# Optimization experiments

Hardware: AMD Instinct MI355X
Metric: run time of the kernel (lower is better)

Reference implementation:

```python
import jax, jax.numpy as jnp
import numpy as np

V, OOV, E, HE, HD, B, S, T = 50000, 100, 128, 256, 256, 32, 256, 16
NEG = -1e20


def lstm(x, W, U, b, h0, c0):
    # x: [B, L, F]; standard (Keras-style i,f,g,o) LSTM via scan over time
    def step(carry, xt):
        h, c = carry
        z = xt @ W + h @ U + b
        i, f, g, o = jnp.split(z, 4, axis=-1)
        c = jax.nn.sigmoid(f) * c + jax.nn.sigmoid(i) * jnp.tanh(g)
        h = jax.nn.sigmoid(o) * jnp.tanh(c)
        return (h, c), h
    (h, c), hs = jax.lax.scan(step, (h0, c0), jnp.swapaxes(x, 0, 1))
    return jnp.swapaxes(hs, 0, 1), h, c


def setup_inputs() -> dict:
    key = jax.random.key(0)
    ks = jax.random.split(key, 16)
    g = lambda i, shape: jax.random.normal(ks[i], shape, dtype=jnp.float32) * 0.05
    return {
        'x': jax.random.randint(ks[0], (B, S), 0, V),
        'x_with_oov': jax.random.randint(ks[1], (B, S), 0, V + OOV),
        'x_len': jax.random.randint(ks[2], (B,), 1, S + 1),
        'dec_x': jax.random.randint(ks[3], (B, T), 0, V),
        'embedding': g(4, (V, E)),
        'Wenc': g(5, (E, 4 * HE)), 'Uenc': g(6, (HE, 4 * HE)), 'benc': jnp.zeros(4 * HE, jnp.float32),
        'We2d': g(7, (HE, HD)), 'be2d': jnp.zeros(HD, jnp.float32),
        'Wdec': g(8, (E, 4 * HD)), 'Udec': g(9, (HD, 4 * HD)), 'bdec': jnp.zeros(4 * HD, jnp.float32),
        'Wattn': g(10, (HD, HE)),
        'Wout': g(11, (HE + HD, HD)), 'bout': jnp.zeros(HD, jnp.float32),
        'Wgen': g(12, (HD, V)),
        'Wcopy': g(13, (HE, HD)), 'bcopy': jnp.zeros(HD, jnp.float32),
    }


def reference(x, x_with_oov, x_len, dec_x, embedding, Wenc, Uenc, benc,
              We2d, be2d, Wdec, Udec, bdec, Wattn, Wout, bout, Wgen, Wcopy, bcopy):
    # Encoder (unidirectional; Keras encoder ignores mask in this branch)
    enc_out, eh, ec = lstm(embedding[x], Wenc, Uenc, benc,
                           jnp.zeros((B, HE), embedding.dtype), jnp.zeros((B, HE), embedding.dtype))
    # NOTE: source applies encoder2decoder_state to BOTH h and c (faithful)
    h0 = eh @ We2d + be2d
    c0 = ec @ We2d + be2d
    # Decoder LSTM
    dec_out, sh, sc = lstm(embedding[dec_x], Wdec, Udec, bdec, h0, c0)  # [B,T,HD]
    mask = jnp.arange(S)[None, :] < x_len[:, None]                      # [B,S]
    # Attention (score_mode='general')
    scores = jnp.einsum('bth,he,bse->bts', dec_out, Wattn, enc_out)     # [B,T,S]
    scores = jnp.where(mask[:, None, :], scores, NEG)
    aw = jax.nn.softmax(scores, axis=2)
    ctx = jnp.einsum('bts,bse->bte', aw, enc_out)                       # [B,T,HE]
    attn_out = jnp.tanh(jnp.concatenate([ctx, dec_out], axis=-1) @ Wout + bout)  # [B,T,HD]
    # Generation scores, padded with tiny constant over OOV slots
    gen = jnp.exp(attn_out @ Wgen)                                      # [B,T,V]
    gen = jnp.pad(gen, ((0, 0), (0, 0), (0, OOV)), constant_values=1e-10)
    # Copy scores over source positions, scattered into extended vocab
    copy_seq = jnp.einsum('bsh,bth->bts', jnp.tanh(enc_out @ Wcopy + bcopy), attn_out)
    copy_seq = jnp.exp(jnp.where(mask[:, None, :], copy_seq, NEG))      # [B,T,S]
    b_idx = jnp.arange(B)[:, None, None]
    t_idx = jnp.arange(T)[None, :, None]
    v_idx = x_with_oov[:, None, :]                                      # broadcast to [B,T,S]
    copy_vocab = jnp.zeros((B, T, V + OOV), gen.dtype).at[b_idx, t_idx, v_idx].add(copy_seq)
    total = gen + copy_vocab
    log_prob = jnp.log(total / jnp.sum(total, axis=2, keepdims=True))
    return log_prob, sh, sc
```

## Files before the change

### kernel.cpp

```cpp
#include <hip/hip_runtime.h>

#define V_   50000
#define OOV_ 100
#define VO_  50100
#define E_   128
#define HE_  256
#define HD_  256
#define B_   32
#define S_   256
#define T_   16

typedef _Float16 h2_t __attribute__((ext_vector_type(2)));
typedef __attribute__((ext_vector_type(8))) short bfrag_t;
typedef __attribute__((ext_vector_type(4))) float f32x4;
typedef unsigned short ushort_t;

union U32H2 { unsigned u; h2_t h; };
union FRAG  { uint4 u; bfrag_t s; };

static __device__ __forceinline__ float bf2f(unsigned short b) {
  return __uint_as_float(((unsigned)b) << 16);
}
static __device__ __forceinline__ unsigned short f2bf(float f) {
  unsigned u = __float_as_uint(f);
  unsigned r = (u + 0x7fffu + ((u >> 16) & 1u)) >> 16;
  return (unsigned short)r;
}
static __device__ __forceinline__ float sigm(float x) { return 1.f / (1.f + expf(-x)); }

static __device__ __forceinline__ float dot2u(unsigned upair, unsigned hpairv, float acc) {
  U32H2 a; a.u = upair;
  U32H2 b; b.u = hpairv;
#if __has_builtin(__builtin_amdgcn_fdot2)
  return __builtin_amdgcn_fdot2(a.h, b.h, acc, false);
#else
  acc = fmaf((float)a.h.x, (float)b.h.x, acc);
  return fmaf((float)a.h.y, (float)b.h.y, acc);
#endif
}

__global__ __launch_bounds__(256) void mfma_gemm(
    const ushort_t* __restrict__ A, const ushort_t* __restrict__ Bt,
    const float* __restrict__ bias, float* __restrict__ C, ushort_t* __restrict__ Cbf,
    float* __restrict__ rsum, int M, int N, int K, int ldC, int act)
{
  const int w = threadIdx.x >> 6, lane = threadIdx.x & 63;
  const int m0 = blockIdx.y * 64 + w * 16;
  const int n0 = blockIdx.x * 64;
  const int l16 = lane & 15, lq = lane >> 4;
  f32x4 acc[4] = {f32x4{0,0,0,0}, f32x4{0,0,0,0}, f32x4{0,0,0,0}, f32x4{0,0,0,0}};
  for (int k0 = 0; k0 < K; k0 += 32) {
    FRAG a;
    a.u = *(const uint4*)(A + (size_t)(m0 + l16) * K + k0 + lq * 8);
#pragma unroll
    for (int ns = 0; ns < 4; ns++) {
      int n = n0 + ns * 16 + l16;
      int nc = n < N ? n : N - 1;
      FRAG bf;
      bf.u = *(const uint4*)(Bt + (size_t)nc * K + k0 + lq * 8);
      acc[ns] = __builtin_amdgcn_mfma_f32_16x16x32_bf16(a.s, bf.s, acc[ns], 0, 0, 0);
    }
  }
  float bv[4];
#pragma unroll
  for (int ns = 0; ns < 4; ns++) {
    int col = n0 + ns * 16 + l16;
    bv[ns] = (bias && col < N) ? bias[col] : 0.f;
  }
#pragma unroll
  for (int r = 0; r < 4; r++) {
    int row = m0 + lq * 4 + r;
    float part = 0.f;
#pragma unroll
    for (int ns = 0; ns < 4; ns++) {
      int col = n0 + ns * 16 + l16;
      if (col < N) {
        float v = acc[ns][r] + bv[ns];
        if (act == 1) v = tanhf(v);
        else if (act == 2) v = expf(v);
        if (Cbf) Cbf[(size_t)row * ldC + col] = f2bf(v);
        else     C[(size_t)row * ldC + col] = v;
        part += v;
      }
    }
    if (rsum) {
      part += __shfl_xor(part, 1);
      part += __shfl_xor(part, 2);
      part += __shfl_xor(part, 4);
      part += __shfl_xor(part, 8);
      if (l16 == 0) atomicAdd(&rsum[row], part);
    }
  }
}

static __device__ __forceinline__ void tconv_tile(
    const float* __restrict__ W, ushort_t* __restrict__ Wt, int K, int N,
    int kb, int nb, int tid, ushort_t (*tile)[33])
{
  const int tx = tid & 31, ty = tid >> 5;
#pragma unroll
  for (int p = 0; p < 4; p++) {
    int k = kb + ty + p * 8, n = nb + tx;
    if (k < K && n < N) tile[ty + p * 8][tx] = f2bf(W[(size_t)k * N + n]);
  }
  __syncthreads();
#pragma unroll
  for (int p = 0; p < 4; p++) {
    int n = nb + ty + p * 8, k = kb + tx;
    if (k < K && n < N) Wt[(size_t)n * K + k] = tile[tx][ty + p * 8];
  }
}
static __device__ __forceinline__ void packU2_one(
    const float* __restrict__ U, unsigned* __restrict__ out, int i)
{
  int p = i >> 10, col = i & 1023;
  U32H2 cv; cv.h = h2_t{(_Float16)U[(size_t)(2 * p) * 1024 + col],
                        (_Float16)U[(size_t)(2 * p + 1) * 1024 + col]};
  out[i] = cv.u;
}

__global__ __launch_bounds__(256) void prep_kernel(
    const float* __restrict__ Wenc, const float* __restrict__ Wdec,
    const float* __restrict__ We2d, const float* __restrict__ Wattn,
    const float* __restrict__ Wout, const float* __restrict__ Wcopy,
    const float* __restrict__ Uenc, const float* __restrict__ Udec,
    const int* __restrict__ x, const int* __restrict__ decx, const float* __restrict__ emb,
    ushort_t* WencT, ushort_t* WdecT, ushort_t* We2dT, ushort_t* WattnT,
    ushort_t* WoutT, ushort_t* WcopyT, unsigned* Upk2E, unsigned* Upk2D,
    ushort_t* xembbf, ushort_t* dembbf)
{
  __shared__ ushort_t tile[32][33];
  int blk = blockIdx.x;
  const int tid = threadIdx.x;
  if (blk < 128) { tconv_tile(Wenc, WencT, 128, 1024, (blk >> 5) * 32, (blk & 31) * 32, tid, tile); return; }
  blk -= 128;
  if (blk < 128) { tconv_tile(Wdec, WdecT, 128, 1024, (blk >> 5) * 32, (blk & 31) * 32, tid, tile); return; }
  blk -= 128;
  if (blk < 64)  { tconv_tile(We2d, We2dT, 256, 256, (blk >> 3) * 32, (blk & 7) * 32, tid, tile); return; }
  blk -= 64;
  if (blk < 64)  { tconv_tile(Wattn, WattnT, 256, 256, (blk >> 3) * 32, (blk & 7) * 32, tid, tile); return; }
  blk -= 64;
  if (blk < 128) { tconv_tile(Wout, WoutT, 512, 256, (blk >> 3) * 32, (blk & 7) * 32, tid, tile); return; }
  blk -= 128;
  if (blk < 64)  { tconv_tile(Wcopy, WcopyT, 256, 256, (blk >> 3) * 32, (blk & 7) * 32, tid, tile); return; }
  blk -= 64;
  if (blk < 512) { packU2_one(Uenc, Upk2E, blk * 256 + tid); return; }
  blk -= 512;
  if (blk < 512) { packU2_one(Udec, Upk2D, blk * 256 + tid); return; }
  blk -= 512;
  if (blk < 4096) {
    int i = blk * 256 + tid, r = i >> 7;
    xembbf[i] = f2bf(emb[(size_t)x[r] * E_ + (i & 127)]);
    return;
  }
  blk -= 4096;
  {
    int i = blk * 256 + tid, r = i >> 7;
    dembbf[i] = f2bf(emb[(size_t)decx[r] * E_ + (i & 127)]);
  }
}

#define DOT8(u0, u1, hpi)                \
  acc[0] = dot2u(u0.x, hpi, acc[0]);     \
  acc[1] = dot2u(u0.y, hpi, acc[1]);     \
  acc[2] = dot2u(u0.z, hpi, acc[2]);     \
  acc[3] = dot2u(u0.w, hpi, acc[3]);     \
  acc[4] = dot2u(u1.x, hpi, acc[4]);     \
  acc[5] = dot2u(u1.y, hpi, acc[5]);     \
  acc[6] = dot2u(u1.z, hpi, acc[6]);     \
  acc[7] = dot2u(u1.w, hpi, acc[7]);

__global__ __launch_bounds__(1024, 4) void lstm4(
    const float* __restrict__ Xpre, const unsigned* __restrict__ Upk2,
    const float* __restrict__ h0, const float* __restrict__ c0,
    ushort_t* __restrict__ outH, float* __restrict__ hN, float* __restrict__ cN,
    int steps, const float* __restrict__ Wg, ushort_t* __restrict__ WgT)
{
  __shared__ unsigned ldsU[32 * 1028];
  __shared__ float zpart[4 * 1028];
  __shared__ float actbuf[1024];
  __shared__ unsigned hpair[128];
  const int tid = threadIdx.x;

  if (blockIdx.x >= 32) {
    ushort_t* tile = (ushort_t*)ldsU;
    int tb = blockIdx.x - 32;
    int kb = (tb & 3) * 64, nb = (tb >> 2) * 64;
#pragma unroll
    for (int p = 0; p < 4; p++) {
      int i = p * 1024 + tid, k = i >> 6, n = i & 63;
      if (nb + n < V_) tile[k * 65 + n] = f2bf(Wg[(size_t)(kb + k) * V_ + nb + n]);
    }
    __syncthreads();
#pragma unroll
    for (int p = 0; p < 4; p++) {
      int i = p * 1024 + tid, n = i >> 6, k = i & 63;
      if (nb + n < V_) WgT[(size_t)(nb + n) * 256 + kb + k] = tile[k * 65 + n];
    }
    return;
  }

  const int b = blockIdx.x;
  const int jg = tid >> 3, kq = tid & 7;

  uint4 Ur[24];
  const unsigned* ubase = Upk2 + jg * 8;
#pragma unroll
  for (int i = 0; i < 12; i++) {
    int p = kq * 16 + i;
    Ur[2 * i]     = *(const uint4*)(ubase + p * 1024);
    Ur[2 * i + 1] = *(const uint4*)(ubase + p * 1024 + 4);
  }
#pragma unroll
  for (int i = 0; i < 4; i++) {
    int p = kq * 16 + 12 + i;
    uint4 q0 = *(const uint4*)(ubase + p * 1024);
    uint4 q1 = *(const uint4*)(ubase + p * 1024 + 4);
    *(uint4*)&ldsU[(kq * 4 + i) * 1028 + jg * 8] = q0;
    *(uint4*)&ldsU[(kq * 4 + i) * 1028 + jg * 8 + 4] = q1;
  }
  float c = 0.f, hcur = 0.f;
  if (tid < 256) {
    c    = c0 ? c0[b * 256 + tid] : 0.f;
    hcur = h0 ? h0[b * 256 + tid] : 0.f;
  }
  if (tid < 128) {
    float a  = h0 ? h0[b * 256 + 2 * tid] : 0.f;
    float b2 = h0 ? h0[b * 256 + 2 * tid + 1] : 0.f;
    U32H2 cv; cv.h = h2_t{(_Float16)a, (_Float16)b2};
    hpair[tid] = cv.u;
  }
  __syncthreads();

  const float* xp = Xpre + (size_t)b * steps * 1024;
  const unsigned* myld = &ldsU[kq * 4 * 1028 + jg * 8];

  for (int t = 0; t < steps; t++) {
    float xv = xp[t * 1024 + tid];
    float acc[8] = {0.f, 0.f, 0.f, 0.f, 0.f, 0.f, 0.f, 0.f};
    {
      uint4 hA = *(const uint4*)&hpair[kq * 16];
      DOT8(Ur[0], Ur[1], hA.x)  DOT8(Ur[2], Ur[3], hA.y)
      DOT8(Ur[4], Ur[5], hA.z)  DOT8(Ur[6], Ur[7], hA.w)
    }
    {
      uint4 hB = *(const uint4*)&hpair[kq * 16 + 4];
      DOT8(Ur[8], Ur[9], hB.x)   DOT8(Ur[10], Ur[11], hB.y)
      DOT8(Ur[12], Ur[13], hB.z) DOT8(Ur[14], Ur[15], hB.w)
    }
    {
      uint4 hC = *(const uint4*)&hpair[kq * 16 + 8];
      DOT8(Ur[16], Ur[17], hC.x) DOT8(Ur[18], Ur[19], hC.y)
      DOT8(Ur[20], Ur[21], hC.z) DOT8(Ur[22], Ur[23], hC.w)
    }
    {
      uint4 hD = *(const uint4*)&hpair[kq * 16 + 12];
      unsigned hh[4] = {hD.x, hD.y, hD.z, hD.w};
#pragma unroll
      for (int r = 0; r < 4; r++) {
        uint4 u0 = *(const uint4*)(myld + r * 1028);
        uint4 u1 = *(const uint4*)(myld + r * 1028 + 4);
        unsigned hpi = hh[r];
        DOT8(u0, u1, hpi)
      }
    }
#pragma unroll
    for (int g = 0; g < 8; g++) acc[g] += __shfl_xor(acc[g], 1);
    if ((kq & 1) == 0) {
      int r = kq >> 1;
      *(float4*)&zpart[r * 1028 + jg * 8]     = make_float4(acc[0], acc[1], acc[2], acc[3]);
      *(float4*)&zpart[r * 1028 + jg * 8 + 4] = make_float4(acc[4], acc[5], acc[6], acc[7]);
    }
    __syncthreads();
    float z = xv + zpart[tid] + zpart[1028 + tid] + zpart[2 * 1028 + tid] + zpart[3 * 1028 + tid];
    actbuf[tid] = (tid >= 512 && tid < 768) ? tanhf(z) : sigm(z);
    __syncthreads();
    if (tid < 256) {
      float ai = actbuf[tid], af = actbuf[tid + 256];
      float gg = actbuf[tid + 512], ao = actbuf[tid + 768];
      c = af * c + ai * gg;
      hcur = ao * tanhf(c);
      outH[((size_t)b * steps + t) * 256 + tid] = f2bf(hcur);
      float hnx = __shfl_down(hcur, 1);
      if ((tid & 1) == 0) {
        U32H2 cv; cv.h = h2_t{(_Float16)hcur, (_Float16)hnx};
        hpair[tid >> 1] = cv.u;
      }
    }
    __syncthreads();
  }
  if (tid < 256) {
    hN[b * 256 + tid] = hcur;
    cN[b * 256 + tid] = c;
  }
}

__global__ __launch_bounds__(256) void attn_kernel(
    const float* __restrict__ dq, const ushort_t* __restrict__ enc,
    const int* __restrict__ x_len, float* __restrict__ ctx)
{
  __shared__ float q[256];
  __shared__ float eb[32][256];
  __shared__ float sc[256];
  __shared__ float red[8];
  const int bt = blockIdx.x, tid = threadIdx.x;
  const int b = bt >> 4;
  q[tid] = dq[(size_t)bt * 256 + tid];
  const int len = x_len[b];
  const unsigned* encu = (const unsigned*)(enc + (size_t)b * S_ * 256);
  __syncthreads();
  const int s_loc = tid >> 3, hb = (tid & 7) * 32;
  for (int cch = 0; cch < 8; cch++) {
#pragma unroll
    for (int qv = 0; qv < 16; qv++) {
      int idx = qv * 256 + tid;
      unsigned u = encu[cch * 4096 + idx];
      int row = idx >> 7, cp2 = (idx & 127) * 2;
      eb[row][cp2]     = bf2f((unsigned short)(u & 0xffffu));
      eb[row][cp2 + 1] = bf2f((unsigned short)(u >> 16));
    }
    __syncthreads();
    float p = 0.f;
#pragma unroll
    for (int h = 0; h < 32; h++) p = fmaf(q[hb + h], eb[s_loc][hb + h], p);
    p += __shfl_down(p, 4, 8);
    p += __shfl_down(p, 2, 8);
    p += __shfl_down(p, 1, 8);
    if ((tid & 7) == 0) sc[cch * 32 + s_loc] = p;
    __syncthreads();
  }
  float my = (tid < len) ? sc[tid] : -1e30f;
  float m = my;
#pragma unroll
  for (int o = 32; o >= 1; o >>= 1) m = fmaxf(m, __shfl_xor(m, o));
  if ((tid & 63) == 0) red[tid >> 6] = m;
  __syncthreads();
  float bm = fmaxf(fmaxf(red[0], red[1]), fmaxf(red[2], red[3]));
  float e = expf(my - bm);
  float s = e;
#pragma unroll
  for (int o = 32; o >= 1; o >>= 1) s += __shfl_xor(s, o);
  if ((tid & 63) == 0) red[4 + (tid >> 6)] = s;
  __syncthreads();
  float tot = red[4] + red[5] + red[6] + red[7];
  sc[tid] = e / tot;
  __syncthreads();
  const ushort_t* encb = enc + (size_t)b * S_ * 256;
// ... 78 lines not shown
  size_t i = (size_t)blockIdx.x * 256 + threadIdx.x;
  if (i < (size_t)B_ * T_ * VO_) {
    int bt = (int)(i / VO_);
    out[i] = logf(out[i]) - rowlog[bt];
  }
}

extern "C" void kernel_launch(void* const* d_in, const int* in_sizes, int n_in,
                              void* d_out, int out_size, void* d_ws, size_t ws_size,
                              hipStream_t stream) {
  const int*   x     = (const int*)d_in[0];
  const int*   xoov  = (const int*)d_in[1];
  const int*   xlen  = (const int*)d_in[2];
  const int*   decx  = (const int*)d_in[3];
  const float* emb   = (const float*)d_in[4];
  const float* Wenc  = (const float*)d_in[5];
  const float* Uenc  = (const float*)d_in[6];
  const float* benc  = (const float*)d_in[7];
  const float* We2d  = (const float*)d_in[8];
  const float* be2d  = (const float*)d_in[9];
  const float* Wdec  = (const float*)d_in[10];
  const float* Udec  = (const float*)d_in[11];
  const float* bdec  = (const float*)d_in[12];
  const float* Wattn = (const float*)d_in[13];
  const float* Wout  = (const float*)d_in[14];
  const float* bout  = (const float*)d_in[15];
  const float* Wgen  = (const float*)d_in[16];
  const float* Wcopy = (const float*)d_in[17];
  const float* bcopy = (const float*)d_in[18];
  float* out = (float*)d_out;
  float* ws  = (float*)d_ws;

  float*    Xenc   = ws + 0;
  ushort_t* WgenT  = (ushort_t*)(ws + 0);
  ushort_t* cp_bf  = (ushort_t*)(ws + 6400000);
  float*    dqb    = ws + 8388608;
  float*    ctxb   = ws + 8519680;
  float*    attno  = ws + 8650752;
  float*    cseq   = ws + 8781824;
  float*    rsum   = ws + 8912896;
  float*    rowlog = ws + 8913408;
  ushort_t* Abf    = (ushort_t*)(ws + 8913920);
  ushort_t* catb   = (ushort_t*)(ws + 8979456);
  ushort_t* decObf = (ushort_t*)(ws + 9110528);
  ushort_t* xembbf = (ushort_t*)(ws + 9176064);
  ushort_t* dembbf = (ushort_t*)(ws + 9700352);
  float*    Xdec   = ws + 9733120;
  ushort_t* WencT  = (ushort_t*)(ws + 10257408);
  ushort_t* WdecT  = (ushort_t*)(ws + 10322944);
  ushort_t* We2dT  = (ushort_t*)(ws + 10388480);
  ushort_t* WattnT = (ushort_t*)(ws + 10421248);
  ushort_t* WoutT  = (ushort_t*)(ws + 10454016);
  ushort_t* WcopyT = (ushort_t*)(ws + 10519552);
  unsigned* Upk2E  = (unsigned*)(ws + 10552320);
  unsigned* Upk2D  = (unsigned*)(ws + 10683392);
  ushort_t* encObf = (ushort_t*)(ws + 10814464);
  float*    ehc    = ws + 11863040;
  ushort_t* ehcbf  = (ushort_t*)(ws + 11879424);
  float*    h0c0   = ws + 11887616;

  float* sh  = out + (size_t)B_ * T_ * VO_;
  float* scf = sh + B_ * HD_;

  hipMemsetAsync(rsum, 0, 512 * sizeof(float), stream);

  hipLaunchKernelGGL(prep_kernel, dim3(5952), dim3(256), 0, stream,
                     Wenc, Wdec, We2d, Wattn, Wout, Wcopy, Uenc, Udec, x, decx, emb,
                     WencT, WdecT, We2dT, WattnT, WoutT, WcopyT, Upk2E, Upk2D,
                     xembbf, dembbf);

  hipLaunchKernelGGL(mfma_gemm, dim3(16, 128), dim3(256), 0, stream,
                     xembbf, WencT, benc, Xenc, (ushort_t*)nullptr, (float*)nullptr,
                     B_ * S_, 1024, 128, 1024, 0);
  hipLaunchKernelGGL(mfma_gemm, dim3(16, 8), dim3(256), 0, stream,
                     dembbf, WdecT, bdec, Xdec, (ushort_t*)nullptr, (float*)nullptr,
                     B_ * T_, 1024, 128, 1024, 0);

  hipLaunchKernelGGL(lstm4, dim3(32), dim3(1024), 0, stream,
                     Xenc, Upk2E, (const float*)nullptr, (const float*)nullptr,
                     encObf, ehc, ehc + 32 * 256, S_,
                     (const float*)nullptr, (ushort_t*)nullptr);

  hipLaunchKernelGGL(f2bf_kernel, dim3(64), dim3(256), 0, stream, ehc, ehcbf, 64 * 256);
  hipLaunchKernelGGL(mfma_gemm, dim3(4, 1), dim3(256), 0, stream,
                     ehcbf, We2dT, be2d, h0c0, (ushort_t*)nullptr, (float*)nullptr,
                     64, 256, 256, 256, 0);

  hipLaunchKernelGGL(lstm4, dim3(32 + 3128), dim3(1024), 0, stream,
                     Xdec, Upk2D, h0c0, h0c0 + 32 * 256, decObf, sh, scf, T_,
                     Wgen, WgenT);

  hipLaunchKernelGGL(mfma_gemm, dim3(4, 8), dim3(256), 0, stream,
                     decObf, WattnT, (const float*)nullptr, dqb, (ushort_t*)nullptr,
                     (float*)nullptr, B_ * T_, 256, 256, 256, 0);
  hipLaunchKernelGGL(attn_kernel, dim3(B_ * T_), dim3(256), 0, stream, dqb, encObf, xlen, ctxb);
  hipLaunchKernelGGL(concat_bf, dim3(1024), dim3(256), 0, stream, ctxb, decObf, catb);
  hipLaunchKernelGGL(mfma_gemm, dim3(4, 8), dim3(256), 0, stream,
                     catb, WoutT, bout, attno, (ushort_t*)nullptr, (float*)nullptr,
                     B_ * T_, 256, 512, 256, 1);
  hipLaunchKernelGGL(f2bf_kernel, dim3(512), dim3(256), 0, stream, attno, Abf, B_ * T_ * 256);
  hipLaunchKernelGGL(mfma_gemm, dim3(4, 128), dim3(256), 0, stream,
                     encObf, WcopyT, bcopy, (float*)nullptr, cp_bf, (float*)nullptr,
                     B_ * S_, 256, 256, 256, 1);
  hipLaunchKernelGGL(mfma_gemm, dim3(782, 8), dim3(256), 0, stream,
                     Abf, WgenT, (const float*)nullptr, out, (ushort_t*)nullptr, rsum,
                     B_ * T_, V_, 256, VO_, 2);
  hipLaunchKernelGGL(pad_kernel, dim3(200), dim3(256), 0, stream, out);
  hipLaunchKernelGGL(copyseq_kernel, dim3(B_ * T_), dim3(256), 0, stream, attno, cp_bf, xlen, cseq);
  hipLaunchKernelGGL(scatter_kernel, dim3(512), dim3(256), 0, stream, cseq, xoov, out, rsum);
  hipLaunchKernelGGL(rowlog_kernel, dim3(2), dim3(256), 0, stream, rsum, rowlog);
  hipLaunchKernelGGL(finalize_kernel, dim3((B_ * T_ * VO_ + 255) / 256), dim3(256), 0, stream,
                     out, rowlog);
}
```

Baseline: 1.215 ms.

## Restructure LSTM recurrence so each thread group owns all four gates of a unit

Repacks the recurrent weight matrix so a quad of threads holds the i/f/g/o columns for one hidden unit, with each thread covering a quarter of the K range. Partial sums are reduced with quad shuffles and the cell update is done in registers, which removes the zpart/actbuf shared-memory round trips. A double-buffered h array cuts the per-step barriers from two to one. tanh is replaced by an exp-based formula, which trades a little accuracy for fewer instructions.

```diff
diff --git a/kernel.cpp b/kernel.cpp
--- a/kernel.cpp
+++ b/kernel.cpp
@@ -27,6 +27,9 @@
   return (unsigned short)r;
 }
 static __device__ __forceinline__ float sigm(float x) { return 1.f / (1.f + expf(-x)); }
+static __device__ __forceinline__ float tanh_fast(float x) {
+  return 2.f / (1.f + expf(-2.f * x)) - 1.f;
+}
 
 static __device__ __forceinline__ float dot2u(unsigned upair, unsigned hpairv, float acc) {
   U32H2 a; a.u = upair;
@@ -113,7 +116,8 @@
 static __device__ __forceinline__ void packU2_one(
     const float* __restrict__ U, unsigned* __restrict__ out, int i)
 {
-  int p = i >> 10, col = i & 1023;
+  int q = i & 3, g = (i >> 2) & 255, p = i >> 10;
+  int col = q * 256 + g;
   U32H2 cv; cv.h = h2_t{(_Float16)U[(size_t)(2 * p) * 1024 + col],
                         (_Float16)U[(size_t)(2 * p + 1) * 1024 + col]};
   out[i] = cv.u;
@@ -160,26 +164,20 @@
   }
 }
 
-#define DOT8(u0, u1, hpi)                \
-  acc[0] = dot2u(u0.x, hpi, acc[0]);     \
-  acc[1] = dot2u(u0.y, hpi, acc[1]);     \
-  acc[2] = dot2u(u0.z, hpi, acc[2]);     \
-  acc[3] = dot2u(u0.w, hpi, acc[3]);     \
-  acc[4] = dot2u(u1.x, hpi, acc[4]);     \
-  acc[5] = dot2u(u1.y, hpi, acc[5]);     \
-  acc[6] = dot2u(u1.z, hpi, acc[6]);     \
-  acc[7] = dot2u(u1.w, hpi, acc[7]);
-
-__global__ __launch_bounds__(1024, 4) void lstm4(
-    const float* __restrict__ Xpre, const unsigned* __restrict__ Upk2,
+#define PSTEP(Uv, hv)                       \
+  acc0 = dot2u((Uv).x, hv, acc0);           \
+  acc1 = dot2u((Uv).y, hv, acc1);           \
+  acc2 = dot2u((Uv).z, hv, acc2);           \
+  acc3 = dot2u((Uv).w, hv, acc3);
+
+__global__ __launch_bounds__(1024, 4) void lstm5(
+    const float* __restrict__ Xpre, const unsigned* __restrict__ Upk,
     const float* __restrict__ h0, const float* __restrict__ c0,
     ushort_t* __restrict__ outH, float* __restrict__ hN, float* __restrict__ cN,
     int steps, const float* __restrict__ Wg, ushort_t* __restrict__ WgT)
 {
-  __shared__ unsigned ldsU[32 * 1028];
-  __shared__ float zpart[4 * 1028];
-  __shared__ float actbuf[1024];
-  __shared__ unsigned hpair[128];
+  __shared__ unsigned ldsU[8 * 4096];
+  __shared__ unsigned hbuf[2][4 * 36];
   const int tid = threadIdx.x;
 
   if (blockIdx.x >= 32) {
@@ -201,97 +199,73 @@
   }
 
   const int b = blockIdx.x;
-  const int jg = tid >> 3, kq = tid & 7;
+  const int g = tid >> 2, r = tid & 3;
 
   uint4 Ur[24];
-  const unsigned* ubase = Upk2 + jg * 8;
-#pragma unroll
-  for (int i = 0; i < 12; i++) {
-    int p = kq * 16 + i;
-    Ur[2 * i]     = *(const uint4*)(ubase + p * 1024);
-    Ur[2 * i + 1] = *(const uint4*)(ubase + p * 1024 + 4);
-  }
-#pragma unroll
-  for (int i = 0; i < 4; i++) {
-    int p = kq * 16 + 12 + i;
-    uint4 q0 = *(const uint4*)(ubase + p * 1024);
-    uint4 q1 = *(const uint4*)(ubase + p * 1024 + 4);
-    *(uint4*)&ldsU[(kq * 4 + i) * 1028 + jg * 8] = q0;
-    *(uint4*)&ldsU[(kq * 4 + i) * 1028 + jg * 8 + 4] = q1;
-  }
-  float c = 0.f, hcur = 0.f;
-  if (tid < 256) {
-    c    = c0 ? c0[b * 256 + tid] : 0.f;
-    hcur = h0 ? h0[b * 256 + tid] : 0.f;
-  }
+  const unsigned* ub = Upk + ((size_t)(r * 32) * 256 + g) * 4;
+#pragma unroll
+  for (int j = 0; j < 24; j++) Ur[j] = *(const uint4*)(ub + j * 1024);
+#pragma unroll
+  for (int j = 0; j < 8; j++)
+    *(uint4*)&ldsU[j * 4096 + tid * 4] = *(const uint4*)(ub + (24 + j) * 1024);
+
+  float c = c0 ? c0[b * 256 + g] : 0.f;
+  float hcur = 0.f;
   if (tid < 128) {
-    float a  = h0 ? h0[b * 256 + 2 * tid] : 0.f;
+    float a  = h0 ? h0[b * 256 + 2 * tid]     : 0.f;
     float b2 = h0 ? h0[b * 256 + 2 * tid + 1] : 0.f;
     U32H2 cv; cv.h = h2_t{(_Float16)a, (_Float16)b2};
-    hpair[tid] = cv.u;
-  }
-  __syncthreads();
-
-  const float* xp = Xpre + (size_t)b * steps * 1024;
-  const unsigned* myld = &ldsU[kq * 4 * 1028 + jg * 8];
-
+    hbuf[0][(tid >> 5) * 36 + (tid & 31)] = cv.u;
+  }
+  __syncthreads();
+
+  const float* xp = Xpre + (size_t)b * steps * 1024 + r * 256 + g;
+  const unsigned* myld = &ldsU[tid * 4];
+
+  int cur = 0;
   for (int t = 0; t < steps; t++) {
-    float xv = xp[t * 1024 + tid];
-    float acc[8] = {0.f, 0.f, 0.f, 0.f, 0.f, 0.f, 0.f, 0.f};
-    {
-      uint4 hA = *(const uint4*)&hpair[kq * 16];
-      DOT8(Ur[0], Ur[1], hA.x)  DOT8(Ur[2], Ur[3], hA.y)
-      DOT8(Ur[4], Ur[5], hA.z)  DOT8(Ur[6], Ur[7], hA.w)
-    }
-    {
-      uint4 hB = *(const uint4*)&hpair[kq * 16 + 4];
-      DOT8(Ur[8], Ur[9], hB.x)   DOT8(Ur[10], Ur[11], hB.y)
-      DOT8(Ur[12], Ur[13], hB.z) DOT8(Ur[14], Ur[15], hB.w)
-    }
-    {
-      uint4 hC = *(const uint4*)&hpair[kq * 16 + 8];
-      DOT8(Ur[16], Ur[17], hC.x) DOT8(Ur[18], Ur[19], hC.y)
-      DOT8(Ur[20], Ur[21], hC.z) DOT8(Ur[22], Ur[23], hC.w)
-    }
-    {
-      uint4 hD = *(const uint4*)&hpair[kq * 16 + 12];
-      unsigned hh[4] = {hD.x, hD.y, hD.z, hD.w};
-#pragma unroll
-      for (int r = 0; r < 4; r++) {
-        uint4 u0 = *(const uint4*)(myld + r * 1028);
-        uint4 u1 = *(const uint4*)(myld + r * 1028 + 4);
-        unsigned hpi = hh[r];
-        DOT8(u0, u1, hpi)
-      }
-    }
-#pragma unroll
-    for (int g = 0; g < 8; g++) acc[g] += __shfl_xor(acc[g], 1);
-    if ((kq & 1) == 0) {
-      int r = kq >> 1;
-      *(float4*)&zpart[r * 1028 + jg * 8]     = make_float4(acc[0], acc[1], acc[2], acc[3]);
-      *(float4*)&zpart[r * 1028 + jg * 8 + 4] = make_float4(acc[4], acc[5], acc[6], acc[7]);
-    }
+    float xv = xp[(size_t)t * 1024];
+    const unsigned* hb = &hbuf[cur][0] + r * 36;
+    float acc0 = 0.f, acc1 = 0.f, acc2 = 0.f, acc3 = 0.f;
+#pragma unroll
+    for (int cc = 0; cc < 6; cc++) {
+      uint4 hp = *(const uint4*)(hb + cc * 4);
+      PSTEP(Ur[4 * cc + 0], hp.x)
+      PSTEP(Ur[4 * cc + 1], hp.y)
+      PSTEP(Ur[4 * cc + 2], hp.z)
+      PSTEP(Ur[4 * cc + 3], hp.w)
+    }
+#pragma unroll
+    for (int j = 0; j < 8; j++) {
+      unsigned hv = hb[24 + j];
+      uint4 uv = *(const uint4*)(myld + j * 4096);
+      PSTEP(uv, hv)
+    }
+    acc0 += (r == 0) ? xv : 0.f;
+    acc1 += (r == 1) ? xv : 0.f;
+    acc2 += (r == 2) ? xv : 0.f;
+    acc3 += (r == 3) ? xv : 0.f;
+    acc0 += __shfl_xor(acc0, 1); acc0 += __shfl_xor(acc0, 2);
+    acc1 += __shfl_xor(acc1, 1); acc1 += __shfl_xor(acc1, 2);
+    acc2 += __shfl_xor(acc2, 1); acc2 += __shfl_xor(acc2, 2);
+    acc3 += __shfl_xor(acc3, 1); acc3 += __shfl_xor(acc3, 2);
+    float ci = sigm(acc0), cf = sigm(acc1);
+    float cg = tanh_fast(acc2), co = sigm(acc3);
+    c = cf * c + ci * cg;
+    hcur = co * tanh_fast(c);
+    if (r == 0) outH[((size_t)b * steps + t) * 256 + g] = f2bf(hcur);
+    float hn = __shfl_down(hcur, 4);
+    if ((tid & 7) == 0) {
+      U32H2 cv; cv.h = h2_t{(_Float16)hcur, (_Float16)hn};
+      int m = tid >> 3;
+      hbuf[cur ^ 1][(m >> 5) * 36 + (m & 31)] = cv.u;
+    }
+    cur ^= 1;
     __syncthreads();
-    float z = xv + zpart[tid] + zpart[1028 + tid] + zpart[2 * 1028 + tid] + zpart[3 * 1028 + tid];
-    actbuf[tid] = (tid >= 512 && tid < 768) ? tanhf(z) : sigm(z);
-    __syncthreads();
-    if (tid < 256) {
-      float ai = actbuf[tid], af = actbuf[tid + 256];
-      float gg = actbuf[tid + 512], ao = actbuf[tid + 768];
-      c = af * c + ai * gg;
-      hcur = ao * tanhf(c);
-      outH[((size_t)b * steps + t) * 256 + tid] = f2bf(hcur);
-      float hnx = __shfl_down(hcur, 1);
-      if ((tid & 1) == 0) {
-        U32H2 cv; cv.h = h2_t{(_Float16)hcur, (_Float16)hnx};
-        hpair[tid >> 1] = cv.u;
-      }
-    }
-    __syncthreads();
-  }
-  if (tid < 256) {
-    hN[b * 256 + tid] = hcur;
-    cN[b * 256 + tid] = c;
+  }
+  if (r == 0) {
+    hN[b * 256 + g] = hcur;
+    cN[b * 256 + g] = c;
   }
 }
 
@@ -501,7 +475,7 @@
                      dembbf, WdecT, bdec, Xdec, (ushort_t*)nullptr, (float*)nullptr,
                      B_ * T_, 1024, 128, 1024, 0);
 
-  hipLaunchKernelGGL(lstm4, dim3(32), dim3(1024), 0, stream,
+  hipLaunchKernelGGL(lstm5, dim3(32), dim3(1024), 0, stream,
                      Xenc, Upk2E, (const float*)nullptr, (const float*)nullptr,
                      encObf, ehc, ehc + 32 * 256, S_,
                      (const float*)nullptr, (ushort_t*)nullptr);
@@ -511,7 +485,7 @@
                      ehcbf, We2dT, be2d, h0c0, (ushort_t*)nullptr, (float*)nullptr,
                      64, 256, 256, 256, 0);
 
-  hipLaunchKernelGGL(lstm4, dim3(32 + 3128), dim3(1024), 0, stream,
+  hipLaunchKernelGGL(lstm5, dim3(32 + 3128), dim3(1024), 0, stream,
                      Xdec, Upk2D, h0c0, h0c0 + 32 * 256, decObf, sh, scf, T_,
                      Wgen, WgenT);
 
```

Result: slower. 1.347 ms (+10.8%).

## Replace dot2 LSTM recurrence with fp16 MFMA over fragment-packed U

Applied to the files above, without the earlier changes.

The per-step h@U product in the LSTM kernel moves from packed fdot2 accumulation with cross-lane shuffles and an LDS partial-sum reduction onto 16x16x32 fp16 MFMA. U is pre-packed into MFMA B-fragment layout, with part held in registers, part in LDS and the rest streamed from global memory each step. The change also prefetches the next step's input pre-activation and swaps expf/tanhf for exp2/rcp approximations. This removes the zpart reduction and a barrier per step, but re-reads part of U from global/L2 every step and broadcasts the batch-1 h vector across MFMA rows, wasting most of each MFMA.

```diff
diff --git a/kernel.cpp b/kernel.cpp
--- a/kernel.cpp
+++ b/kernel.cpp
@@ -12,11 +12,13 @@
 
 typedef _Float16 h2_t __attribute__((ext_vector_type(2)));
 typedef __attribute__((ext_vector_type(8))) short bfrag_t;
+typedef _Float16 hfrag_t __attribute__((ext_vector_type(8)));
 typedef __attribute__((ext_vector_type(4))) float f32x4;
 typedef unsigned short ushort_t;
 
 union U32H2 { unsigned u; h2_t h; };
 union FRAG  { uint4 u; bfrag_t s; };
+union FRAGH { uint4 u; hfrag_t h; };
 
 static __device__ __forceinline__ float bf2f(unsigned short b) {
   return __uint_as_float(((unsigned)b) << 16);
@@ -26,18 +28,10 @@
   unsigned r = (u + 0x7fffu + ((u >> 16) & 1u)) >> 16;
   return (unsigned short)r;
 }
+static __device__ __forceinline__ ushort_t f2h(float f) {
+  union { _Float16 h; ushort_t u; } cv; cv.h = (_Float16)f; return cv.u;
+}
 static __device__ __forceinline__ float sigm(float x) { return 1.f / (1.f + expf(-x)); }
-
-static __device__ __forceinline__ float dot2u(unsigned upair, unsigned hpairv, float acc) {
-  U32H2 a; a.u = upair;
-  U32H2 b; b.u = hpairv;
-#if __has_builtin(__builtin_amdgcn_fdot2)
-  return __builtin_amdgcn_fdot2(a.h, b.h, acc, false);
-#else
-  acc = fmaf((float)a.h.x, (float)b.h.x, acc);
-  return fmaf((float)a.h.y, (float)b.h.y, acc);
-#endif
-}
 
 __global__ __launch_bounds__(256) void mfma_gemm(
     const ushort_t* __restrict__ A, const ushort_t* __restrict__ Bt,
@@ -110,13 +104,13 @@
     if (k < K && n < N) Wt[(size_t)n * K + k] = tile[tx][ty + p * 8];
   }
 }
-static __device__ __forceinline__ void packU2_one(
-    const float* __restrict__ U, unsigned* __restrict__ out, int i)
-{
-  int p = i >> 10, col = i & 1023;
-  U32H2 cv; cv.h = h2_t{(_Float16)U[(size_t)(2 * p) * 1024 + col],
-                        (_Float16)U[(size_t)(2 * p + 1) * 1024 + col]};
-  out[i] = cv.u;
+static __device__ __forceinline__ void packUfrag_one(
+    const float* __restrict__ U, ushort_t* __restrict__ out, int i)
+{
+  int e = i & 7, l = (i >> 3) & 63, ntg = (i >> 9) & 63, kk = i >> 15;
+  int col = ntg * 16 + (l & 15);
+  int k = kk * 32 + (l >> 4) * 8 + e;
+  out[i] = f2h(U[(size_t)k * 1024 + col]);
 }
 
 __global__ __launch_bounds__(256) void prep_kernel(
@@ -126,7 +120,7 @@
     const float* __restrict__ Uenc, const float* __restrict__ Udec,
     const int* __restrict__ x, const int* __restrict__ decx, const float* __restrict__ emb,
     ushort_t* WencT, ushort_t* WdecT, ushort_t* We2dT, ushort_t* WattnT,
-    ushort_t* WoutT, ushort_t* WcopyT, unsigned* Upk2E, unsigned* Upk2D,
+    ushort_t* WoutT, ushort_t* WcopyT, ushort_t* UfragE, ushort_t* UfragD,
     ushort_t* xembbf, ushort_t* dembbf)
 {
   __shared__ ushort_t tile[32][33];
@@ -144,10 +138,10 @@
   blk -= 128;
   if (blk < 64)  { tconv_tile(Wcopy, WcopyT, 256, 256, (blk >> 3) * 32, (blk & 7) * 32, tid, tile); return; }
   blk -= 64;
-  if (blk < 512) { packU2_one(Uenc, Upk2E, blk * 256 + tid); return; }
-  blk -= 512;
-  if (blk < 512) { packU2_one(Udec, Upk2D, blk * 256 + tid); return; }
-  blk -= 512;
+  if (blk < 1024) { packUfrag_one(Uenc, UfragE, blk * 256 + tid); return; }
+  blk -= 1024;
+  if (blk < 1024) { packUfrag_one(Udec, UfragD, blk * 256 + tid); return; }
+  blk -= 1024;
   if (blk < 4096) {
     int i = blk * 256 + tid, r = i >> 7;
     xembbf[i] = f2bf(emb[(size_t)x[r] * E_ + (i & 127)]);
@@ -160,30 +154,19 @@
   }
 }
 
-#define DOT8(u0, u1, hpi)                \
-  acc[0] = dot2u(u0.x, hpi, acc[0]);     \
-  acc[1] = dot2u(u0.y, hpi, acc[1]);     \
-  acc[2] = dot2u(u0.z, hpi, acc[2]);     \
-  acc[3] = dot2u(u0.w, hpi, acc[3]);     \
-  acc[4] = dot2u(u1.x, hpi, acc[4]);     \
-  acc[5] = dot2u(u1.y, hpi, acc[5]);     \
-  acc[6] = dot2u(u1.z, hpi, acc[6]);     \
-  acc[7] = dot2u(u1.w, hpi, acc[7]);
-
-__global__ __launch_bounds__(1024, 4) void lstm4(
-    const float* __restrict__ Xpre, const unsigned* __restrict__ Upk2,
+__global__ __launch_bounds__(1024, 4) void lstm6(
+    const float* __restrict__ Xpre, const ushort_t* __restrict__ Ufrag,
     const float* __restrict__ h0, const float* __restrict__ c0,
     ushort_t* __restrict__ outH, float* __restrict__ hN, float* __restrict__ cN,
     int steps, const float* __restrict__ Wg, ushort_t* __restrict__ WgT)
 {
-  __shared__ unsigned ldsU[32 * 1028];
-  __shared__ float zpart[4 * 1028];
-  __shared__ float actbuf[1024];
-  __shared__ unsigned hpair[128];
+  __shared__ __align__(16) ushort_t ldsB[2 * 64 * 64 * 8];
+  __shared__ float actb[1024];
+  __shared__ __align__(16) ushort_t hH[256];
   const int tid = threadIdx.x;
 
   if (blockIdx.x >= 32) {
-    ushort_t* tile = (ushort_t*)ldsU;
+    ushort_t* tile = ldsB;
     int tb = blockIdx.x - 32;
     int kb = (tb & 3) * 64, nb = (tb >> 2) * 64;
 #pragma unroll
@@ -201,98 +184,105 @@
   }
 
   const int b = blockIdx.x;
-  const int jg = tid >> 3, kq = tid & 7;
-
-  uint4 Ur[24];
-  const unsigned* ubase = Upk2 + jg * 8;
-#pragma unroll
-  for (int i = 0; i < 12; i++) {
-    int p = kq * 16 + i;
-    Ur[2 * i]     = *(const uint4*)(ubase + p * 1024);
-    Ur[2 * i + 1] = *(const uint4*)(ubase + p * 1024 + 4);
-  }
-#pragma unroll
-  for (int i = 0; i < 4; i++) {
-    int p = kq * 16 + 12 + i;
-    uint4 q0 = *(const uint4*)(ubase + p * 1024);
-    uint4 q1 = *(const uint4*)(ubase + p * 1024 + 4);
-    *(uint4*)&ldsU[(kq * 4 + i) * 1028 + jg * 8] = q0;
-    *(uint4*)&ldsU[(kq * 4 + i) * 1028 + jg * 8 + 4] = q1;
-  }
+  const int w = tid >> 6, l = tid & 63;
+  const int lq = l >> 4, lq8 = lq * 8, w4 = w * 4;
+
+  const ushort_t* p0 = Ufrag + (size_t)w4 * 512 + l * 8;
+
+  FRAGH Br[12];
+#pragma unroll
+  for (int kk = 0; kk < 3; kk++)
+#pragma unroll
+    for (int j = 0; j < 4; j++)
+      Br[kk * 4 + j].u = *(const uint4*)(p0 + kk * 32768 + j * 512);
+#pragma unroll
+  for (int kk = 3; kk < 5; kk++)
+#pragma unroll
+    for (int j = 0; j < 4; j++) {
+      uint4 v = *(const uint4*)(p0 + kk * 32768 + j * 512);
+      *(uint4*)&ldsB[(size_t)(((kk - 3) * 64 + w4 + j) * 64 + l) * 8] = v;
+    }
+
   float c = 0.f, hcur = 0.f;
   if (tid < 256) {
     c    = c0 ? c0[b * 256 + tid] : 0.f;
     hcur = h0 ? h0[b * 256 + tid] : 0.f;
-  }
-  if (tid < 128) {
-    float a  = h0 ? h0[b * 256 + 2 * tid] : 0.f;
-    float b2 = h0 ? h0[b * 256 + 2 * tid + 1] : 0.f;
-    U32H2 cv; cv.h = h2_t{(_Float16)a, (_Float16)b2};
-    hpair[tid] = cv.u;
-  }
-  __syncthreads();
-
+    hH[tid] = f2h(hcur);
+  }
   const float* xp = Xpre + (size_t)b * steps * 1024;
-  const unsigned* myld = &ldsU[kq * 4 * 1028 + jg * 8];
+  float xv = xp[tid];
+  __syncthreads();
+
+#define KK_MFMA(KKI, B0, B1, B2, B3)                                              \
+  { FRAGH ah_; ah_.u = *(const uint4*)&hH[(KKI) * 32 + lq8];                      \
+    acc0 = __builtin_amdgcn_mfma_f32_16x16x32_f16(ah_.h, (B0).h, acc0, 0, 0, 0);  \
+    acc1 = __builtin_amdgcn_mfma_f32_16x16x32_f16(ah_.h, (B1).h, acc1, 0, 0, 0);  \
+    acc2 = __builtin_amdgcn_mfma_f32_16x16x32_f16(ah_.h, (B2).h, acc2, 0, 0, 0);  \
+    acc3 = __builtin_amdgcn_mfma_f32_16x16x32_f16(ah_.h, (B3).h, acc3, 0, 0, 0); }
 
   for (int t = 0; t < steps; t++) {
-    float xv = xp[t * 1024 + tid];
-    float acc[8] = {0.f, 0.f, 0.f, 0.f, 0.f, 0.f, 0.f, 0.f};
+    float xvn = xp[(size_t)((t + 1 < steps) ? t + 1 : t) * 1024 + tid];
+    f32x4 acc0 = f32x4{0,0,0,0}, acc1 = f32x4{0,0,0,0},
+          acc2 = f32x4{0,0,0,0}, acc3 = f32x4{0,0,0,0};
+    FRAGH g5[4], g6[4], g7[4];
+#pragma unroll
+    for (int j = 0; j < 4; j++) g5[j].u = *(const uint4*)(p0 + 5 * 32768 + j * 512);
+#pragma unroll
+    for (int j = 0; j < 4; j++) g6[j].u = *(const uint4*)(p0 + 6 * 32768 + j * 512);
+    KK_MFMA(0, Br[0], Br[1], Br[2], Br[3])
+    KK_MFMA(1, Br[4], Br[5], Br[6], Br[7])
+    KK_MFMA(2, Br[8], Br[9], Br[10], Br[11])
+    KK_MFMA(5, g5[0], g5[1], g5[2], g5[3])
+#pragma unroll
+    for (int j = 0; j < 4; j++) g7[j].u = *(const uint4*)(p0 + 7 * 32768 + j * 512);
+    KK_MFMA(6, g6[0], g6[1], g6[2], g6[3])
     {
-      uint4 hA = *(const uint4*)&hpair[kq * 16];
-      DOT8(Ur[0], Ur[1], hA.x)  DOT8(Ur[2], Ur[3], hA.y)
-      DOT8(Ur[4], Ur[5], hA.z)  DOT8(Ur[6], Ur[7], hA.w)
-    }
+      FRAGH b0, b1, b2, b3;
+      b0.u = *(const uint4*)&ldsB[(size_t)((0 * 64 + w4 + 0) * 64 + l) * 8];
+      b1.u = *(const uint4*)&ldsB[(size_t)((0 * 64 + w4 + 1) * 64 + l) * 8];
+      b2.u = *(const uint4*)&ldsB[(size_t)((0 * 64 + w4 + 2) * 64 + l) * 8];
+      b3.u = *(const uint4*)&ldsB[(size_t)((0 * 64 + w4 + 3) * 64 + l) * 8];
+      KK_MFMA(3, b0, b1, b2, b3)
+    }
+    KK_MFMA(7, g7[0], g7[1], g7[2], g7[3])
     {
-      uint4 hB = *(const uint4*)&hpair[kq * 16 + 4];
-      DOT8(Ur[8], Ur[9], hB.x)   DOT8(Ur[10], Ur[11], hB.y)
-      DOT8(Ur[12], Ur[13], hB.z) DOT8(Ur[14], Ur[15], hB.w)
-    }
-    {
-      uint4 hC = *(const uint4*)&hpair[kq * 16 + 8];
-      DOT8(Ur[16], Ur[17], hC.x) DOT8(Ur[18], Ur[19], hC.y)
-      DOT8(Ur[20], Ur[21], hC.z) DOT8(Ur[22], Ur[23], hC.w)
-    }
-    {
-      uint4 hD = *(const uint4*)&hpair[kq * 16 + 12];
-      unsigned hh[4] = {hD.x, hD.y, hD.z, hD.w};
-#pragma unroll
-      for (int r = 0; r < 4; r++) {
-        uint4 u0 = *(const uint4*)(myld + r * 1028);
-        uint4 u1 = *(const uint4*)(myld + r * 1028 + 4);
-        unsigned hpi = hh[r];
-        DOT8(u0, u1, hpi)
-      }
-    }
-#pragma unroll
-    for (int g = 0; g < 8; g++) acc[g] += __shfl_xor(acc[g], 1);
-    if ((kq & 1) == 0) {
-      int r = kq >> 1;
-      *(float4*)&zpart[r * 1028 + jg * 8]     = make_float4(acc[0], acc[1], acc[2], acc[3]);
-      *(float4*)&zpart[r * 1028 + jg * 8 + 4] = make_float4(acc[4], acc[5], acc[6], acc[7]);
-    }
-    __syncthreads();
-    float z = xv + zpart[tid] + zpart[1028 + tid] + zpart[2 * 1028 + tid] + zpart[3 * 1028 + tid];
-    actbuf[tid] = (tid >= 512 && tid < 768) ? tanhf(z) : sigm(z);
+      FRAGH b0, b1, b2, b3;
+      b0.u = *(const uint4*)&ldsB[(size_t)((1 * 64 + w4 + 0) * 64 + l) * 8];
+      b1.u = *(const uint4*)&ldsB[(size_t)((1 * 64 + w4 + 1) * 64 + l) * 8];
+      b2.u = *(const uint4*)&ldsB[(size_t)((1 * 64 + w4 + 2) * 64 + l) * 8];
+      b3.u = *(const uint4*)&ldsB[(size_t)((1 * 64 + w4 + 3) * 64 + l) * 8];
+      KK_MFMA(4, b0, b1, b2, b3)
+    }
+    float z = (lq == 0) ? acc0[0] : (lq == 1) ? acc1[0] : (lq == 2) ? acc2[0] : acc3[0];
+    z += xv;
+    float av;
+    if (w >= 8 && w < 12) {
+      float e = __builtin_amdgcn_exp2f(-2.885390082f * z);
+      av = 2.f * __builtin_amdgcn_rcpf(1.f + e) - 1.f;
+    } else {
+      float e = __builtin_amdgcn_exp2f(-1.442695041f * z);
+      av = __builtin_amdgcn_rcpf(1.f + e);
+    }
+    actb[tid] = av;
     __syncthreads();
     if (tid < 256) {
-      float ai = actbuf[tid], af = actbuf[tid + 256];
-      float gg = actbuf[tid + 512], ao = actbuf[tid + 768];
-      c = af * c + ai * gg;
-      hcur = ao * tanhf(c);
+      float ai = actb[tid], af = actb[256 + tid];
+      float ag = actb[512 + tid], ao = actb[768 + tid];
+      c = fmaf(af, c, ai * ag);
+      float e2 = __builtin_amdgcn_exp2f(-2.885390082f * c);
+      float th = 2.f * __builtin_amdgcn_rcpf(1.f + e2) - 1.f;
+      hcur = ao * th;
       outH[((size_t)b * steps + t) * 256 + tid] = f2bf(hcur);
-      float hnx = __shfl_down(hcur, 1);
-      if ((tid & 1) == 0) {
-        U32H2 cv; cv.h = h2_t{(_Float16)hcur, (_Float16)hnx};
-        hpair[tid >> 1] = cv.u;
-      }
-    }
+      hH[tid] = f2h(hcur);
+    }
+    xv = xvn;
     __syncthreads();
   }
   if (tid < 256) {
     hN[b * 256 + tid] = hcur;
     cN[b * 256 + tid] = c;
   }
+#undef KK_MFMA
 }
 
 __global__ __launch_bounds__(256) void attn_kernel(
@@ -477,8 +467,8 @@
   ushort_t* WattnT = (ushort_t*)(ws + 10421248);
   ushort_t* WoutT  = (ushort_t*)(ws + 10454016);
   ushort_t* WcopyT = (ushort_t*)(ws + 10519552);
-  unsigned* Upk2E  = (unsigned*)(ws + 10552320);
-  unsigned* Upk2D  = (unsigned*)(ws + 10683392);
+  ushort_t* UfragE = (ushort_t*)(ws + 10552320);
+  ushort_t* UfragD = (ushort_t*)(ws + 10683392);
   ushort_t* encObf = (ushort_t*)(ws + 10814464);
   float*    ehc    = ws + 11863040;
   ushort_t* ehcbf  = (ushort_t*)(ws + 11879424);
@@ -489,9 +479,9 @@
 
   hipMemsetAsync(rsum, 0, 512 * sizeof(float), stream);
 
-  hipLaunchKernelGGL(prep_kernel, dim3(5952), dim3(256), 0, stream,
+  hipLaunchKernelGGL(prep_kernel, dim3(6976), dim3(256), 0, stream,
                      Wenc, Wdec, We2d, Wattn, Wout, Wcopy, Uenc, Udec, x, decx, emb,
-                     WencT, WdecT, We2dT, WattnT, WoutT, WcopyT, Upk2E, Upk2D,
+                     WencT, WdecT, We2dT, WattnT, WoutT, WcopyT, UfragE, UfragD,
                      xembbf, dembbf);
 
   hipLaunchKernelGGL(mfma_gemm, dim3(16, 128), dim3(256), 0, stream,
@@ -501,8 +491,8 @@
                      dembbf, WdecT, bdec, Xdec, (ushort_t*)nullptr, (float*)nullptr,
                      B_ * T_, 1024, 128, 1024, 0);
 
-  hipLaunchKernelGGL(lstm4, dim3(32), dim3(1024), 0, stream,
-                     Xenc, Upk2E, (const float*)nullptr, (const float*)nullptr,
+  hipLaunchKernelGGL(lstm6, dim3(32), dim3(1024), 0, stream,
+                     Xenc, UfragE, (const float*)nullptr, (const float*)nullptr,
                      encObf, ehc, ehc + 32 * 256, S_,
                      (const float*)nullptr, (ushort_t*)nullptr);
 
@@ -511,8 +501,8 @@
                      ehcbf, We2dT, be2d, h0c0, (ushort_t*)nullptr, (float*)nullptr,
                      64, 256, 256, 256, 0);
 
-  hipLaunchKernelGGL(lstm4, dim3(32 + 3128), dim3(1024), 0, stream,
-                     Xdec, Upk2D, h0c0, h0c0 + 32 * 256, decObf, sh, scf, T_,
+  hipLaunchKernelGGL(lstm6, dim3(32 + 3128), dim3(1024), 0, stream,
+                     Xdec, UfragD, h0c0, h0c0 + 32 * 256, decObf, sh, scf, T_,
                      Wgen, WgenT);
 
   hipLaunchKernelGGL(mfma_gemm, dim3(4, 8), dim3(256), 0, stream,
```

Result: slower. 1.415 ms (+16.5%).

## Replicate LSTM cell update per wave to drop the third barrier per step

Applied to the files above, without the earlier changes.

The LSTM step kernel now has every wave compute the full cell update (4 units per lane) redundantly and write its own private padded copy of the packed hidden state. This removes the third __syncthreads per timestep and the single-wave tail where only 256 threads worked. Activations switch to hardware exp2/rcp intrinsics, and LDS layouts are re-padded to avoid bank conflicts. The cost is 16x redundant cell math, extra LDS for the hidden buffers, and slightly lower-precision transcendentals.

```diff
diff --git a/kernel.cpp b/kernel.cpp
--- a/kernel.cpp
+++ b/kernel.cpp
@@ -25,6 +25,9 @@
   unsigned u = __float_as_uint(f);
   unsigned r = (u + 0x7fffu + ((u >> 16) & 1u)) >> 16;
   return (unsigned short)r;
+}
+static __device__ __forceinline__ unsigned packh2(float a, float b) {
+  U32H2 cv; cv.h = h2_t{(_Float16)a, (_Float16)b}; return cv.u;
 }
 static __device__ __forceinline__ float sigm(float x) { return 1.f / (1.f + expf(-x)); }
 
@@ -170,16 +173,16 @@
   acc[6] = dot2u(u1.z, hpi, acc[6]);     \
   acc[7] = dot2u(u1.w, hpi, acc[7]);
 
-__global__ __launch_bounds__(1024, 4) void lstm4(
+__global__ __launch_bounds__(1024, 4) void lstm7(
     const float* __restrict__ Xpre, const unsigned* __restrict__ Upk2,
     const float* __restrict__ h0, const float* __restrict__ c0,
     ushort_t* __restrict__ outH, float* __restrict__ hN, float* __restrict__ cN,
     int steps, const float* __restrict__ Wg, ushort_t* __restrict__ WgT)
 {
-  __shared__ unsigned ldsU[32 * 1028];
-  __shared__ float zpart[4 * 1028];
-  __shared__ float actbuf[1024];
-  __shared__ unsigned hpair[128];
+  __shared__ unsigned ldsU[8 * 4113];
+  __shared__ float    zpart[4 * 1026];
+  __shared__ float    actb[1024];
+  __shared__ unsigned hbuf[16 * 136];
   const int tid = threadIdx.x;
 
   if (blockIdx.x >= 32) {
@@ -202,6 +205,7 @@
 
   const int b = blockIdx.x;
   const int jg = tid >> 3, kq = tid & 7;
+  const int wv = tid >> 6, lane = tid & 63;
 
   uint4 Ur[24];
   const unsigned* ubase = Upk2 + jg * 8;
@@ -216,51 +220,53 @@
     int p = kq * 16 + 12 + i;
     uint4 q0 = *(const uint4*)(ubase + p * 1024);
     uint4 q1 = *(const uint4*)(ubase + p * 1024 + 4);
-    *(uint4*)&ldsU[(kq * 4 + i) * 1028 + jg * 8] = q0;
-    *(uint4*)&ldsU[(kq * 4 + i) * 1028 + jg * 8 + 4] = q1;
-  }
-  float c = 0.f, hcur = 0.f;
-  if (tid < 256) {
-    c    = c0 ? c0[b * 256 + tid] : 0.f;
-    hcur = h0 ? h0[b * 256 + tid] : 0.f;
-  }
-  if (tid < 128) {
-    float a  = h0 ? h0[b * 256 + 2 * tid] : 0.f;
-    float b2 = h0 ? h0[b * 256 + 2 * tid + 1] : 0.f;
-    U32H2 cv; cv.h = h2_t{(_Float16)a, (_Float16)b2};
-    hpair[tid] = cv.u;
+    *(uint4*)&ldsU[kq * 4113 + i * 1028 + jg * 8]     = q0;
+    *(uint4*)&ldsU[kq * 4113 + i * 1028 + jg * 8 + 4] = q1;
+  }
+
+  float c4[4] = {0.f, 0.f, 0.f, 0.f};
+  float h4[4] = {0.f, 0.f, 0.f, 0.f};
+  if (c0) { float4 cv = *(const float4*)&c0[b * 256 + 4 * lane];
+            c4[0] = cv.x; c4[1] = cv.y; c4[2] = cv.z; c4[3] = cv.w; }
+  {
+    float4 hv = make_float4(0.f, 0.f, 0.f, 0.f);
+    if (h0) hv = *(const float4*)&h0[b * 256 + 4 * lane];
+    int p0 = 2 * lane;
+    hbuf[wv * 136 + p0 + (p0 >> 4)]           = packh2(hv.x, hv.y);
+    hbuf[wv * 136 + (p0 + 1) + ((p0 + 1) >> 4)] = packh2(hv.z, hv.w);
   }
   __syncthreads();
 
   const float* xp = Xpre + (size_t)b * steps * 1024;
-  const unsigned* myld = &ldsU[kq * 4 * 1028 + jg * 8];
+  const unsigned* myld = &ldsU[kq * 4113 + jg * 8];
+  const unsigned* hb = &hbuf[wv * 136 + kq * 17];
 
   for (int t = 0; t < steps; t++) {
-    float xv = xp[t * 1024 + tid];
+    float xv = xp[(size_t)t * 1024 + tid];
     float acc[8] = {0.f, 0.f, 0.f, 0.f, 0.f, 0.f, 0.f, 0.f};
     {
-      uint4 hA = *(const uint4*)&hpair[kq * 16];
+      uint4 hA = *(const uint4*)&hb[0];
       DOT8(Ur[0], Ur[1], hA.x)  DOT8(Ur[2], Ur[3], hA.y)
       DOT8(Ur[4], Ur[5], hA.z)  DOT8(Ur[6], Ur[7], hA.w)
     }
     {
-      uint4 hB = *(const uint4*)&hpair[kq * 16 + 4];
+      uint4 hB = *(const uint4*)&hb[4];
       DOT8(Ur[8], Ur[9], hB.x)   DOT8(Ur[10], Ur[11], hB.y)
       DOT8(Ur[12], Ur[13], hB.z) DOT8(Ur[14], Ur[15], hB.w)
     }
     {
-      uint4 hC = *(const uint4*)&hpair[kq * 16 + 8];
+      uint4 hC = *(const uint4*)&hb[8];
       DOT8(Ur[16], Ur[17], hC.x) DOT8(Ur[18], Ur[19], hC.y)
       DOT8(Ur[20], Ur[21], hC.z) DOT8(Ur[22], Ur[23], hC.w)
     }
     {
-      uint4 hD = *(const uint4*)&hpair[kq * 16 + 12];
+      uint4 hD = *(const uint4*)&hb[12];
       unsigned hh[4] = {hD.x, hD.y, hD.z, hD.w};
 #pragma unroll
-      for (int r = 0; r < 4; r++) {
-        uint4 u0 = *(const uint4*)(myld + r * 1028);
-        uint4 u1 = *(const uint4*)(myld + r * 1028 + 4);
-        unsigned hpi = hh[r];
+      for (int i = 0; i < 4; i++) {
+        uint4 u0 = *(const uint4*)(myld + i * 1028);
+        uint4 u1 = *(const uint4*)(myld + i * 1028 + 4);
+        unsigned hpi = hh[i];
         DOT8(u0, u1, hpi)
       }
     }
@@ -268,30 +274,52 @@
     for (int g = 0; g < 8; g++) acc[g] += __shfl_xor(acc[g], 1);
     if ((kq & 1) == 0) {
       int r = kq >> 1;
-      *(float4*)&zpart[r * 1028 + jg * 8]     = make_float4(acc[0], acc[1], acc[2], acc[3]);
-      *(float4*)&zpart[r * 1028 + jg * 8 + 4] = make_float4(acc[4], acc[5], acc[6], acc[7]);
-    }
-    __syncthreads();
-    float z = xv + zpart[tid] + zpart[1028 + tid] + zpart[2 * 1028 + tid] + zpart[3 * 1028 + tid];
-    actbuf[tid] = (tid >= 512 && tid < 768) ? tanhf(z) : sigm(z);
-    __syncthreads();
-    if (tid < 256) {
-      float ai = actbuf[tid], af = actbuf[tid + 256];
-      float gg = actbuf[tid + 512], ao = actbuf[tid + 768];
-      c = af * c + ai * gg;
-      hcur = ao * tanhf(c);
-      outH[((size_t)b * steps + t) * 256 + tid] = f2bf(hcur);
-      float hnx = __shfl_down(hcur, 1);
-      if ((tid & 1) == 0) {
-        U32H2 cv; cv.h = h2_t{(_Float16)hcur, (_Float16)hnx};
-        hpair[tid >> 1] = cv.u;
+      *(float4*)&zpart[r * 1026 + jg * 8]     = make_float4(acc[0], acc[1], acc[2], acc[3]);
+      *(float4*)&zpart[r * 1026 + jg * 8 + 4] = make_float4(acc[4], acc[5], acc[6], acc[7]);
+    }
+    __syncthreads();
+    {
+      float z = xv + zpart[tid] + zpart[1026 + tid] + zpart[2052 + tid] + zpart[3078 + tid];
+      float av;
+      if (tid >= 512 && tid < 768) {
+        float e = __builtin_amdgcn_exp2f(-2.885390082f * z);
+        av = 2.f * __builtin_amdgcn_rcpf(1.f + e) - 1.f;
+      } else {
+        float e = __builtin_amdgcn_exp2f(-1.442695041f * z);
+        av = __builtin_amdgcn_rcpf(1.f + e);
       }
-    }
-    __syncthreads();
-  }
-  if (tid < 256) {
-    hN[b * 256 + tid] = hcur;
-    cN[b * 256 + tid] = c;
+      actb[tid] = av;
+    }
+    __syncthreads();
+    {
+      float4 I = *(const float4*)&actb[4 * lane];
+      float4 F = *(const float4*)&actb[256 + 4 * lane];
+      float4 G = *(const float4*)&actb[512 + 4 * lane];
+      float4 O = *(const float4*)&actb[768 + 4 * lane];
+      float iv[4] = {I.x, I.y, I.z, I.w};
+      float fv[4] = {F.x, F.y, F.z, F.w};
+      float gv[4] = {G.x, G.y, G.z, G.w};
+      float ov[4] = {O.x, O.y, O.z, O.w};
+#pragma unroll
+      for (int j = 0; j < 4; j++) {
+        c4[j] = fmaf(fv[j], c4[j], iv[j] * gv[j]);
+        float e2 = __builtin_amdgcn_exp2f(-2.885390082f * c4[j]);
+        float th = 2.f * __builtin_amdgcn_rcpf(1.f + e2) - 1.f;
+        h4[j] = ov[j] * th;
+      }
+      int p0 = 2 * lane;
+      hbuf[wv * 136 + p0 + (p0 >> 4)]             = packh2(h4[0], h4[1]);
+      hbuf[wv * 136 + (p0 + 1) + ((p0 + 1) >> 4)] = packh2(h4[2], h4[3]);
+      if (wv == 0) {
+        unsigned lo = (unsigned)f2bf(h4[0]) | ((unsigned)f2bf(h4[1]) << 16);
+        unsigned hi = (unsigned)f2bf(h4[2]) | ((unsigned)f2bf(h4[3]) << 16);
+        *(uint2*)&outH[((size_t)b * steps + t) * 256 + 4 * lane] = make_uint2(lo, hi);
+      }
+    }
+  }
+  if (wv == 0) {
+    *(float4*)&hN[b * 256 + 4 * lane] = make_float4(h4[0], h4[1], h4[2], h4[3]);
+    *(float4*)&cN[b * 256 + 4 * lane] = make_float4(c4[0], c4[1], c4[2], c4[3]);
   }
 }
 
@@ -501,7 +529,7 @@
                      dembbf, WdecT, bdec, Xdec, (ushort_t*)nullptr, (float*)nullptr,
                      B_ * T_, 1024, 128, 1024, 0);
 
-  hipLaunchKernelGGL(lstm4, dim3(32), dim3(1024), 0, stream,
+  hipLaunchKernelGGL(lstm7, dim3(32), dim3(1024), 0, stream,
                      Xenc, Upk2E, (const float*)nullptr, (const float*)nullptr,
                      encObf, ehc, ehc + 32 * 256, S_,
                      (const float*)nullptr, (ushort_t*)nullptr);
@@ -511,7 +539,7 @@
                      ehcbf, We2dT, be2d, h0c0, (ushort_t*)nullptr, (float*)nullptr,
                      64, 256, 256, 256, 0);
 
-  hipLaunchKernelGGL(lstm4, dim3(32 + 3128), dim3(1024), 0, stream,
+  hipLaunchKernelGGL(lstm7, dim3(32 + 3128), dim3(1024), 0, stream,
                      Xdec, Upk2D, h0c0, h0c0 + 32 * 256, decObf, sh, scf, T_,
                      Wgen, WgenT);
 
```

New measurement: 2.315 ms. 90.5% more time.
